# Optimization experiments

Hardware: AMD Instinct MI355X
Metric: run time of the kernel (lower is better)

## Reference

```python
import jax, jax.numpy as jnp
import numpy as np
from jax import lax

D_MODEL = 32
N_HEADS = 8
QS = 24       # query_shape
FLANGE = 8    # memory_flange


def _conv3x3(x, w, b=None):
    y = lax.conv_general_dilated(x, w, (1, 1), 'SAME',
                                 dimension_numbers=('NCHW', 'OIHW', 'NCHW'))
    if b is not None:
        y = y + b[None, :, None, None]
    return y


def _forward(x, q_w, q_b, k_w, k_b, v_w, v_b, out_w):
    B, Cin, H, W0 = x.shape
    nh, dm, qs, fl = N_HEADS, D_MODEL, QS, FLANGE
    c = dm // nh  # depth per head (=4)

    q = _conv3x3(x, q_w, q_b)
    k = _conv3x3(x, k_w, k_b)
    v = _conv3x3(x, v_w, v_b)

    pad = (-W0) % qs
    if pad:
        p = ((0, 0), (0, 0), (0, 0), (0, pad))
        q = jnp.pad(q, p); k = jnp.pad(k, p); v = jnp.pad(v, p)
    T = q.shape[-1]
    M = T // qs
    F = 2 * fl + qs  # window length (=40)

    q = q.reshape(B, nh, c, H, T) * (c ** -0.5)
    k = jnp.pad(k.reshape(B, nh, c, H, T), ((0, 0),) * 4 + ((fl, fl),))
    v = jnp.pad(v.reshape(B, nh, c, H, T), ((0, 0),) * 4 + ((fl, fl),))

    # Faithful reproduction of torch.as_strided(k, shape, unfold_q.stride()):
    # the source uses q's (contiguous, time-length T) strides on k/v whose
    # storage rows have length T+2*fl, so we gather by storage-linear index.
    s0, s1, s2, s3 = nh * c * H * T, c * H * T, H * T, T
    idx = (jnp.arange(B)[:, None, None, None, None, None] * s0
           + jnp.arange(nh)[:, None, None, None, None] * s1
           + jnp.arange(c)[:, None, None, None] * s2
           + jnp.arange(H)[:, None, None] * s3
           + jnp.arange(M)[:, None] * qs
           + jnp.arange(F))  # (B,nh,c,H,M,F)
    uk = k.reshape(-1)[idx]
    uv = v.reshape(-1)[idx]

    qq = q.reshape(B, nh, c, H, M, qs).transpose(0, 1, 4, 3, 5, 2)
    qq = qq.reshape(B * nh * M, H * qs, c)                     # (G, H*qs, c)
    k2 = uk.transpose(0, 1, 4, 2, 3, 5).reshape(B * nh * M, c, H * F)
    v2 = uv.transpose(0, 1, 4, 3, 5, 2).reshape(B * nh * M, H * F, c)

    # note: source uses -1e-09 (not -1e9); reproduced exactly
    bias = (jnp.sum(jnp.abs(k2), axis=-2, keepdims=True) == 0).astype(k2.dtype) * (-1e-09)
    weights = jax.nn.softmax(qq @ k2 + bias, axis=-1)
    o = weights @ v2                                            # (G, H*qs, c)

    o = o.reshape(B, nh, M, H, qs, c).transpose(0, 1, 5, 3, 2, 4)
    o = o.reshape(B, dm, H, M * qs)[..., :H, :W0]
    return _conv3x3(o, out_w)


def setup_inputs() -> dict:
    key = jax.random.key(0)
    ks = jax.random.split(key, 8)
    B, Cin, H, W = 2, 64, 32, 192
    s = 0.05
    return {
        'x': jax.random.normal(ks[0], (B, Cin, H, W), jnp.float32),
        'q_w': jax.random.normal(ks[1], (D_MODEL, Cin, 3, 3), jnp.float32) * s,
        'q_b': jax.random.normal(ks[2], (D_MODEL,), jnp.float32) * s,
        'k_w': jax.random.normal(ks[3], (D_MODEL, Cin, 3, 3), jnp.float32) * s,
        'k_b': jax.random.normal(ks[4], (D_MODEL,), jnp.float32) * s,
        'v_w': jax.random.normal(ks[5], (D_MODEL, Cin, 3, 3), jnp.float32) * s,
        'v_b': jax.random.normal(ks[6], (D_MODEL,), jnp.float32) * s,
        'out_w': jax.random.normal(ks[7], (64, D_MODEL, 3, 3), jnp.float32) * s,
    }


def reference(x, q_w, q_b, k_w, k_b, v_w, v_b, out_w):
    return _forward(x, q_w, q_b, k_w, k_b, v_w, v_b, out_w)
```

## Files before the change

### kernel.cpp

```cpp
#include <hip/hip_runtime.h>

namespace {
constexpr int B   = 2;
constexpr int CIN = 64;
constexpr int H   = 32;
constexpr int W   = 192;
constexpr int DM  = 32;
constexpr int NH  = 8;
constexpr int C   = 4;
constexpr int QS  = 24;
constexpr int FL  = 8;
constexpr int T   = 192;
constexpr int TP  = T + 2 * FL;
constexpr int M   = T / QS;
constexpr int F   = 2 * FL + QS;
constexpr int HF  = H * F;
constexpr int JC  = HF / 4;
constexpr int WP  = W + 2;
constexpr int HWP = H * WP;

constexpr size_t XP_OFF  = 0;
constexpr size_t KVI_OFF = 0;
constexpr size_t Q_OFF   = 1310720;
constexpr size_t K_OFF   = Q_OFF + 393216;
constexpr size_t V_OFF   = K_OFF + 425984;
constexpr size_t O_OFF   = K_OFF;
constexpr size_t ZR_OFF  = V_OFF + 425984;

constexpr int S0 = NH * C * H * T;
constexpr int S1 = C * H * T;
constexpr int S2 = H * T;
constexpr int S3 = T;
}

__global__ __launch_bounds__(256) void prep_x_k(const float* __restrict__ x,
                                                float* __restrict__ ws) {
  int row = blockIdx.x;
  int c = threadIdx.x;
  if (c >= WP) return;
  float v = (c == 0 || c == WP - 1) ? 0.f : x[(size_t)row * W + (c - 1)];
  ws[XP_OFF + (size_t)row * WP + c] = v;
}

__global__ __launch_bounds__(256) void zero_pads_k(float* __restrict__ ws) {
  int t = blockIdx.x * 256 + threadIdx.x;
  if (t < 32768) {
    int row = t >> 4;
    int p = t & 15;
    int col = (p < 8) ? p : (192 + p);
    size_t addr = (size_t)row * TP + col;
    ws[K_OFF + addr] = 0.f;
    ws[V_OFF + addr] = 0.f;
  } else if (t < 32768 + 256) {
    ws[ZR_OFF + (t - 32768)] = 0.f;
  }
}

__global__ __launch_bounds__(192) void qkv_conv_k(
    const float* __restrict__ qw, const float* __restrict__ qb,
    const float* __restrict__ kw, const float* __restrict__ kb,
    const float* __restrict__ vw, const float* __restrict__ vb,
    float* __restrict__ ws) {
  int bid = blockIdx.x;
  int y  = bid & 31;
  int co = (bid >> 5) & 31;
  int b  = bid >> 10;
  int xp = threadIdx.x;

  const float* zr  = ws + ZR_OFF;
  const float* xpb = ws + XP_OFF + (size_t)b * CIN * HWP;

  const float* p0; const float* p1; const float* p2;
  int st0, st2;
  p1 = xpb + y * WP;
  if (y > 0)     { p0 = xpb + (y - 1) * WP; st0 = HWP; } else { p0 = zr; st0 = 0; }
  if (y < H - 1) { p2 = xpb + (y + 1) * WP; st2 = HWP; } else { p2 = zr; st2 = 0; }

  const float* wq = qw + co * (CIN * 9);
  const float* wk = kw + co * (CIN * 9);
  const float* wv = vw + co * (CIN * 9);
  float aq = qb[co], ak = kb[co], av = vb[co];

#pragma unroll 2
  for (int ci = 0; ci < CIN; ++ci) {
    float a0 = p0[xp], a1 = p0[xp + 1], a2 = p0[xp + 2];
    float b0 = p1[xp], b1 = p1[xp + 1], b2 = p1[xp + 2];
    float c0 = p2[xp], c1 = p2[xp + 1], c2 = p2[xp + 2];

    aq = fmaf(a0, wq[0], aq); ak = fmaf(a0, wk[0], ak); av = fmaf(a0, wv[0], av);
    aq = fmaf(a1, wq[1], aq); ak = fmaf(a1, wk[1], ak); av = fmaf(a1, wv[1], av);
    aq = fmaf(a2, wq[2], aq); ak = fmaf(a2, wk[2], ak); av = fmaf(a2, wv[2], av);
    aq = fmaf(b0, wq[3], aq); ak = fmaf(b0, wk[3], ak); av = fmaf(b0, wv[3], av);
    aq = fmaf(b1, wq[4], aq); ak = fmaf(b1, wk[4], ak); av = fmaf(b1, wv[4], av);
    aq = fmaf(b2, wq[5], aq); ak = fmaf(b2, wk[5], ak); av = fmaf(b2, wv[5], av);
    aq = fmaf(c0, wq[6], aq); ak = fmaf(c0, wk[6], ak); av = fmaf(c0, wv[6], av);
    aq = fmaf(c1, wq[7], aq); ak = fmaf(c1, wk[7], ak); av = fmaf(c1, wv[7], av);
    aq = fmaf(c2, wq[8], aq); ak = fmaf(c2, wk[8], ak); av = fmaf(c2, wv[8], av);

    p0 += st0; p1 += HWP; p2 += st2;
    wq += 9; wk += 9; wv += 9;
  }

  ws[Q_OFF + ((size_t)(b * DM + co) * H + y) * T + xp] = aq;
  int h = co >> 2, c4 = co & 3;
  size_t pa = ((size_t)((b * NH + h) * C + c4) * H + y) * TP + FL + xp;
  ws[K_OFF + pa] = ak;
  ws[V_OFF + pa] = av;
}

__global__ __launch_bounds__(256) void build_kv_k(float* __restrict__ ws) {
  const float* kp = ws + K_OFF;
  const float* vp = ws + V_OFF;
  float* kvi = ws + KVI_OFF;
  int t = blockIdx.x * 256 + threadIdx.x;
  int c  = t & 7;
  int gj = t >> 3;
  int g  = gj / HF;
  int j  = gj - g * HF;
  int b = g >> 6, h = (g >> 3) & 7, m = g & 7;
  int hh = j / F, f = j - hh * F;
  int ci = c & 3;
  const float* src = (c < 4) ? kp : vp;
  int addr = b * S0 + h * S1 + ci * S2 + hh * S3 + m * QS + f;
  kvi[t] = src[addr];
}

__global__ __launch_bounds__(256) void attn_k(float* __restrict__ ws) {
  const float* qbuf = ws + Q_OFF;
  const float* kvi  = ws + KVI_OFF;
  float*       ob   = ws + O_OFF;

  int g  = blockIdx.x;
  int rb = blockIdx.y;
  int b = g >> 6, h = (g >> 3) & 7, m = g & 7;
  int tid = threadIdx.x;
  int row = tid & 63;
  int jc  = __builtin_amdgcn_readfirstlane(tid >> 6);

  int r  = rb * 64 + row;
  int hh = r / QS, qi = r - hh * QS;
  size_t qidx = (((size_t)(b * DM + h * C) * H + hh) * T) + m * QS + qi;
  float q0 = qbuf[qidx]             * 0.5f;
  float q1 = qbuf[qidx + H * T]     * 0.5f;
  float q2 = qbuf[qidx + 2 * H * T] * 0.5f;
  float q3 = qbuf[qidx + 3 * H * T] * 0.5f;

  const float* kvp = kvi + ((size_t)g * HF + (size_t)jc * JC) * 8;

  float s = 0.f, o0 = 0.f, o1 = 0.f, o2 = 0.f, o3 = 0.f;
#pragma unroll 4
  for (int j = 0; j < JC; ++j) {
    float4 k4 = *reinterpret_cast<const float4*>(kvp + j * 8);
    float4 v4 = *reinterpret_cast<const float4*>(kvp + j * 8 + 4);
    float l = fmaf(q0, k4.x, fmaf(q1, k4.y, fmaf(q2, k4.z, q3 * k4.w)));
    float e = __expf(l);
    s += e;
    o0 = fmaf(e, v4.x, o0);
    o1 = fmaf(e, v4.y, o1);
    o2 = fmaf(e, v4.z, o2);
    o3 = fmaf(e, v4.w, o3);
  }

  __shared__ float red[4][64][5];
  red[jc][row][0] = s;
  red[jc][row][1] = o0;
  red[jc][row][2] = o1;
  red[jc][row][3] = o2;
  red[jc][row][4] = o3;
  __syncthreads();

  if (tid < 64) {
    float S = 0.f, O0 = 0.f, O1 = 0.f, O2 = 0.f, O3 = 0.f;
#pragma unroll
    for (int cx = 0; cx < 4; ++cx) {
      S  += red[cx][tid][0];
      O0 += red[cx][tid][1];
      O1 += red[cx][tid][2];
      O2 += red[cx][tid][3];
      O3 += red[cx][tid][4];
    }
    float inv = 1.0f / S;
    size_t obase = (((size_t)(b * DM + h * C) * H + hh) * WP) + 1 + m * QS + qi;
    ob[obase]            = O0 * inv;
    ob[obase + HWP]      = O1 * inv;
    ob[obase + 2 * HWP]  = O2 * inv;
    ob[obase + 3 * HWP]  = O3 * inv;
    if (m == 0 && qi == 0) {
      ob[obase - 1] = 0.f; ob[obase - 1 + HWP] = 0.f;
      ob[obase - 1 + 2 * HWP] = 0.f; ob[obase - 1 + 3 * HWP] = 0.f;
    }
    if (m == M - 1 && qi == QS - 1) {
      ob[obase + 1] = 0.f; ob[obase + 1 + HWP] = 0.f;
      ob[obase + 1 + 2 * HWP] = 0.f; ob[obase + 1 + 3 * HWP] = 0.f;
    }
  }
}

__global__ __launch_bounds__(192) void out_conv_k(const float* __restrict__ ws,
                                                  const float* __restrict__ ow,
                                                  float* __restrict__ out) {
  int bid = blockIdx.x;
  int y  = bid & 31;
  int cq = (bid >> 5) & 15;
  int b  = bid >> 9;
  int xp = threadIdx.x;

  const float* zr  = ws + ZR_OFF;
  const float* obb = ws + O_OFF + (size_t)b * DM * HWP;

  const float* p0; const float* p1; const float* p2;
  int st0, st2;
  p1 = obb + y * WP;
  if (y > 0)     { p0 = obb + (y - 1) * WP; st0 = HWP; } else { p0 = zr; st0 = 0; }
  if (y < H - 1) { p2 = obb + (y + 1) * WP; st2 = HWP; } else { p2 = zr; st2 = 0; }

  int co0 = cq * 4;
  const float* w0 = ow + (size_t)(co0 + 0) * (DM * 9);
  const float* w1 = ow + (size_t)(co0 + 1) * (DM * 9);
  const float* w2 = ow + (size_t)(co0 + 2) * (DM * 9);
  const float* w3 = ow + (size_t)(co0 + 3) * (DM * 9);
  float A0 = 0.f, A1 = 0.f, A2 = 0.f, A3 = 0.f;

#pragma unroll 2
  for (int ci = 0; ci < DM; ++ci) {
    float a0 = p0[xp], a1 = p0[xp + 1], a2 = p0[xp + 2];
    float b0 = p1[xp], b1 = p1[xp + 1], b2 = p1[xp + 2];
    float c0 = p2[xp], c1 = p2[xp + 1], c2 = p2[xp + 2];

    A0 = fmaf(a0, w0[0], A0); A1 = fmaf(a0, w1[0], A1); A2 = fmaf(a0, w2[0], A2); A3 = fmaf(a0, w3[0], A3);
    A0 = fmaf(a1, w0[1], A0); A1 = fmaf(a1, w1[1], A1); A2 = fmaf(a1, w2[1], A2); A3 = fmaf(a1, w3[1], A3);
    A0 = fmaf(a2, w0[2], A0); A1 = fmaf(a2, w1[2], A1); A2 = fmaf(a2, w2[2], A2); A3 = fmaf(a2, w3[2], A3);
    A0 = fmaf(b0, w0[3], A0); A1 = fmaf(b0, w1[3], A1); A2 = fmaf(b0, w2[3], A2); A3 = fmaf(b0, w3[3], A3);
    A0 = fmaf(b1, w0[4], A0); A1 = fmaf(b1, w1[4], A1); A2 = fmaf(b1, w2[4], A2); A3 = fmaf(b1, w3[4], A3);
    A0 = fmaf(b2, w0[5], A0); A1 = fmaf(b2, w1[5], A1); A2 = fmaf(b2, w2[5], A2); A3 = fmaf(b2, w3[5], A3);
    A0 = fmaf(c0, w0[6], A0); A1 = fmaf(c0, w1[6], A1); A2 = fmaf(c0, w2[6], A2); A3 = fmaf(c0, w3[6], A3);
    A0 = fmaf(c1, w0[7], A0); A1 = fmaf(c1, w1[7], A1); A2 = fmaf(c1, w2[7], A2); A3 = fmaf(c1, w3[7], A3);
    A0 = fmaf(c2, w0[8], A0); A1 = fmaf(c2, w1[8], A1); A2 = fmaf(c2, w2[8], A2); A3 = fmaf(c2, w3[8], A3);

    p0 += st0; p1 += HWP; p2 += st2;
    w0 += 9; w1 += 9; w2 += 9; w3 += 9;
  }

  size_t ob0 = ((size_t)(b * 64 + co0) * H + y) * W + xp;
  out[ob0]           = A0;
  out[ob0 + H * W]   = A1;
  out[ob0 + 2*H*W]   = A2;
  out[ob0 + 3*H*W]   = A3;
}

extern "C" void kernel_launch(void* const* d_in, const int* in_sizes, int n_in,
                              void* d_out, int out_size, void* d_ws, size_t ws_size,
                              hipStream_t stream) {
  const float* x  = (const float*)d_in[0];
  const float* qw = (const float*)d_in[1];
  const float* qb = (const float*)d_in[2];
  const float* kw = (const float*)d_in[3];
  const float* kb = (const float*)d_in[4];
  const float* vw = (const float*)d_in[5];
  const float* vb = (const float*)d_in[6];
  const float* ow = (const float*)d_in[7];
  float* out = (float*)d_out;
  float* ws  = (float*)d_ws;

  hipLaunchKernelGGL(prep_x_k,   dim3(B * CIN * H), dim3(256), 0, stream, x, ws);
  hipLaunchKernelGGL(zero_pads_k, dim3(130), dim3(256), 0, stream, ws);
  hipLaunchKernelGGL(qkv_conv_k, dim3(B * 32 * 32), dim3(192), 0, stream,
                     qw, qb, kw, kb, vw, vb, ws);
  hipLaunchKernelGGL(build_kv_k, dim3(5120), dim3(256), 0, stream, ws);
  hipLaunchKernelGGL(attn_k,     dim3(128, 12), dim3(256), 0, stream, ws);
  hipLaunchKernelGGL(out_conv_k, dim3(B * 16 * 32), dim3(192), 0, stream, ws, ow, out);
}
```

Measured before the change: 117.6 us.

## Register-block conv kernels over 4 output pixels and merge prep launches

Both 3x3 conv kernels now have each thread compute four adjacent output columns. Each thread loads its input rows with float4/float2 vector reads and writes results with float4 stores. The padded row width becomes 196 so the vector loads stay aligned. The x-padding and zero-pad kernels are merged into one launch to cut launch overhead. The conv grids shrink to 512 blocks, which lowers parallelism and occupancy in exchange for reusing inputs from registers and issuing fewer memory instructions.

```diff
diff --git a/kernel.cpp b/kernel.cpp
--- a/kernel.cpp
+++ b/kernel.cpp
@@ -16,7 +16,7 @@
 constexpr int F   = 2 * FL + QS;
 constexpr int HF  = H * F;
 constexpr int JC  = HF / 4;
-constexpr int WP  = W + 2;
+constexpr int WP  = 196;
 constexpr int HWP = H * WP;
 
 constexpr size_t XP_OFF  = 0;
@@ -33,26 +33,25 @@
 constexpr int S3 = T;
 }
 
-__global__ __launch_bounds__(256) void prep_x_k(const float* __restrict__ x,
-                                                float* __restrict__ ws) {
-  int row = blockIdx.x;
-  int c = threadIdx.x;
-  if (c >= WP) return;
-  float v = (c == 0 || c == WP - 1) ? 0.f : x[(size_t)row * W + (c - 1)];
-  ws[XP_OFF + (size_t)row * WP + c] = v;
-}
-
-__global__ __launch_bounds__(256) void zero_pads_k(float* __restrict__ ws) {
-  int t = blockIdx.x * 256 + threadIdx.x;
-  if (t < 32768) {
+__global__ __launch_bounds__(256) void prep_k(const float* __restrict__ x,
+                                              float* __restrict__ ws) {
+  int bid = blockIdx.x;
+  int tid = threadIdx.x;
+  if (bid < 4096) {
+    if (tid < WP) {
+      float v = (tid >= 1 && tid <= W) ? x[(size_t)bid * W + (tid - 1)] : 0.f;
+      ws[XP_OFF + (size_t)bid * WP + tid] = v;
+    }
+  } else if (bid < 4224) {
+    int t = (bid - 4096) * 256 + tid;
     int row = t >> 4;
     int p = t & 15;
     int col = (p < 8) ? p : (192 + p);
     size_t addr = (size_t)row * TP + col;
     ws[K_OFF + addr] = 0.f;
     ws[V_OFF + addr] = 0.f;
-  } else if (t < 32768 + 256) {
-    ws[ZR_OFF + (t - 32768)] = 0.f;
+  } else {
+    ws[ZR_OFF + tid] = 0.f;
   }
 }
 
@@ -62,50 +61,67 @@
     const float* __restrict__ vw, const float* __restrict__ vb,
     float* __restrict__ ws) {
   int bid = blockIdx.x;
-  int y  = bid & 31;
-  int co = (bid >> 5) & 31;
-  int b  = bid >> 10;
-  int xp = threadIdx.x;
+  int yq = bid & 7;
+  int co = (bid >> 3) & 31;
+  int b  = bid >> 8;
+  int tid = threadIdx.x;
+  int yl = tid / 48;
+  int xq = tid - yl * 48;
+  int y  = yq * 4 + yl;
+  int xp = xq * 4;
 
   const float* zr  = ws + ZR_OFF;
   const float* xpb = ws + XP_OFF + (size_t)b * CIN * HWP;
 
-  const float* p0; const float* p1; const float* p2;
-  int st0, st2;
-  p1 = xpb + y * WP;
-  if (y > 0)     { p0 = xpb + (y - 1) * WP; st0 = HWP; } else { p0 = zr; st0 = 0; }
-  if (y < H - 1) { p2 = xpb + (y + 1) * WP; st2 = HWP; } else { p2 = zr; st2 = 0; }
+  const float* p0 = (y > 0)     ? xpb + (y - 1) * WP + xp : zr + xp;
+  const float* p1 = xpb + y * WP + xp;
+  const float* p2 = (y < H - 1) ? xpb + (y + 1) * WP + xp : zr + xp;
+  int st0 = (y > 0)     ? HWP : 0;
+  int st2 = (y < H - 1) ? HWP : 0;
 
   const float* wq = qw + co * (CIN * 9);
   const float* wk = kw + co * (CIN * 9);
   const float* wv = vw + co * (CIN * 9);
-  float aq = qb[co], ak = kb[co], av = vb[co];
+
+  float q0b = qb[co], k0b = kb[co], v0b = vb[co];
+  float Aq[4] = {q0b, q0b, q0b, q0b};
+  float Ak[4] = {k0b, k0b, k0b, k0b};
+  float Av[4] = {v0b, v0b, v0b, v0b};
 
 #pragma unroll 2
   for (int ci = 0; ci < CIN; ++ci) {
-    float a0 = p0[xp], a1 = p0[xp + 1], a2 = p0[xp + 2];
-    float b0 = p1[xp], b1 = p1[xp + 1], b2 = p1[xp + 2];
-    float c0 = p2[xp], c1 = p2[xp + 1], c2 = p2[xp + 2];
-
-    aq = fmaf(a0, wq[0], aq); ak = fmaf(a0, wk[0], ak); av = fmaf(a0, wv[0], av);
-    aq = fmaf(a1, wq[1], aq); ak = fmaf(a1, wk[1], ak); av = fmaf(a1, wv[1], av);
-    aq = fmaf(a2, wq[2], aq); ak = fmaf(a2, wk[2], ak); av = fmaf(a2, wv[2], av);
-    aq = fmaf(b0, wq[3], aq); ak = fmaf(b0, wk[3], ak); av = fmaf(b0, wv[3], av);
-    aq = fmaf(b1, wq[4], aq); ak = fmaf(b1, wk[4], ak); av = fmaf(b1, wv[4], av);
-    aq = fmaf(b2, wq[5], aq); ak = fmaf(b2, wk[5], ak); av = fmaf(b2, wv[5], av);
-    aq = fmaf(c0, wq[6], aq); ak = fmaf(c0, wk[6], ak); av = fmaf(c0, wv[6], av);
-    aq = fmaf(c1, wq[7], aq); ak = fmaf(c1, wk[7], ak); av = fmaf(c1, wv[7], av);
-    aq = fmaf(c2, wq[8], aq); ak = fmaf(c2, wk[8], ak); av = fmaf(c2, wv[8], av);
-
+    float4 a4 = *reinterpret_cast<const float4*>(p0);
+    float2 a2 = *reinterpret_cast<const float2*>(p0 + 4);
+    float4 b4 = *reinterpret_cast<const float4*>(p1);
+    float2 b2 = *reinterpret_cast<const float2*>(p1 + 4);
+    float4 c4 = *reinterpret_cast<const float4*>(p2);
+    float2 c2 = *reinterpret_cast<const float2*>(p2 + 4);
+    float av_[6] = {a4.x, a4.y, a4.z, a4.w, a2.x, a2.y};
+    float bv_[6] = {b4.x, b4.y, b4.z, b4.w, b2.x, b2.y};
+    float cv_[6] = {c4.x, c4.y, c4.z, c4.w, c2.x, c2.y};
+#pragma unroll
+    for (int dx = 0; dx < 3; ++dx) {
+      float wq0 = wq[dx], wq1 = wq[3 + dx], wq2 = wq[6 + dx];
+      float wk0 = wk[dx], wk1 = wk[3 + dx], wk2 = wk[6 + dx];
+      float wv0 = wv[dx], wv1 = wv[3 + dx], wv2 = wv[6 + dx];
+#pragma unroll
+      for (int o = 0; o < 4; ++o) {
+        float xa = av_[o + dx], xb = bv_[o + dx], xc = cv_[o + dx];
+        Aq[o] = fmaf(xa, wq0, Aq[o]); Aq[o] = fmaf(xb, wq1, Aq[o]); Aq[o] = fmaf(xc, wq2, Aq[o]);
+        Ak[o] = fmaf(xa, wk0, Ak[o]); Ak[o] = fmaf(xb, wk1, Ak[o]); Ak[o] = fmaf(xc, wk2, Ak[o]);
+        Av[o] = fmaf(xa, wv0, Av[o]); Av[o] = fmaf(xb, wv1, Av[o]); Av[o] = fmaf(xc, wv2, Av[o]);
+      }
+    }
     p0 += st0; p1 += HWP; p2 += st2;
     wq += 9; wk += 9; wv += 9;
   }
 
-  ws[Q_OFF + ((size_t)(b * DM + co) * H + y) * T + xp] = aq;
-  int h = co >> 2, c4 = co & 3;
-  size_t pa = ((size_t)((b * NH + h) * C + c4) * H + y) * TP + FL + xp;
-  ws[K_OFF + pa] = ak;
-  ws[V_OFF + pa] = av;
+  *reinterpret_cast<float4*>(ws + Q_OFF + ((size_t)(b * DM + co) * H + y) * T + xp) =
+      make_float4(Aq[0], Aq[1], Aq[2], Aq[3]);
+  int h = co >> 2, c4i = co & 3;
+  size_t pa = ((size_t)((b * NH + h) * C + c4i) * H + y) * TP + FL + xp;
+  *reinterpret_cast<float4*>(ws + K_OFF + pa) = make_float4(Ak[0], Ak[1], Ak[2], Ak[3]);
+  *reinterpret_cast<float4*>(ws + V_OFF + pa) = make_float4(Av[0], Av[1], Av[2], Av[3]);
 }
 
 __global__ __launch_bounds__(256) void build_kv_k(float* __restrict__ ws) {
@@ -200,52 +216,59 @@
                                                   const float* __restrict__ ow,
                                                   float* __restrict__ out) {
   int bid = blockIdx.x;
-  int y  = bid & 31;
-  int cq = (bid >> 5) & 15;
-  int b  = bid >> 9;
-  int xp = threadIdx.x;
+  int yq = bid & 7;
+  int cp = (bid >> 3) & 31;
+  int b  = bid >> 8;
+  int tid = threadIdx.x;
+  int yl = tid / 48;
+  int xq = tid - yl * 48;
+  int y  = yq * 4 + yl;
+  int xp = xq * 4;
 
   const float* zr  = ws + ZR_OFF;
   const float* obb = ws + O_OFF + (size_t)b * DM * HWP;
 
-  const float* p0; const float* p1; const float* p2;
-  int st0, st2;
-  p1 = obb + y * WP;
-  if (y > 0)     { p0 = obb + (y - 1) * WP; st0 = HWP; } else { p0 = zr; st0 = 0; }
-  if (y < H - 1) { p2 = obb + (y + 1) * WP; st2 = HWP; } else { p2 = zr; st2 = 0; }
-
-  int co0 = cq * 4;
-  const float* w0 = ow + (size_t)(co0 + 0) * (DM * 9);
-  const float* w1 = ow + (size_t)(co0 + 1) * (DM * 9);
-  const float* w2 = ow + (size_t)(co0 + 2) * (DM * 9);
-  const float* w3 = ow + (size_t)(co0 + 3) * (DM * 9);
-  float A0 = 0.f, A1 = 0.f, A2 = 0.f, A3 = 0.f;
+  const float* p0 = (y > 0)     ? obb + (y - 1) * WP + xp : zr + xp;
+  const float* p1 = obb + y * WP + xp;
+  const float* p2 = (y < H - 1) ? obb + (y + 1) * WP + xp : zr + xp;
+  int st0 = (y > 0)     ? HWP : 0;
+  int st2 = (y < H - 1) ? HWP : 0;
+
+  int co0 = cp * 2;
+  const float* w0 = ow + (size_t)co0 * (DM * 9);
+  const float* w1 = w0 + DM * 9;
+  float A0[4] = {0.f, 0.f, 0.f, 0.f};
+  float A1[4] = {0.f, 0.f, 0.f, 0.f};
 
 #pragma unroll 2
   for (int ci = 0; ci < DM; ++ci) {
-    float a0 = p0[xp], a1 = p0[xp + 1], a2 = p0[xp + 2];
-    float b0 = p1[xp], b1 = p1[xp + 1], b2 = p1[xp + 2];
-    float c0 = p2[xp], c1 = p2[xp + 1], c2 = p2[xp + 2];
-
-    A0 = fmaf(a0, w0[0], A0); A1 = fmaf(a0, w1[0], A1); A2 = fmaf(a0, w2[0], A2); A3 = fmaf(a0, w3[0], A3);
-    A0 = fmaf(a1, w0[1], A0); A1 = fmaf(a1, w1[1], A1); A2 = fmaf(a1, w2[1], A2); A3 = fmaf(a1, w3[1], A3);
-    A0 = fmaf(a2, w0[2], A0); A1 = fmaf(a2, w1[2], A1); A2 = fmaf(a2, w2[2], A2); A3 = fmaf(a2, w3[2], A3);
-    A0 = fmaf(b0, w0[3], A0); A1 = fmaf(b0, w1[3], A1); A2 = fmaf(b0, w2[3], A2); A3 = fmaf(b0, w3[3], A3);
-    A0 = fmaf(b1, w0[4], A0); A1 = fmaf(b1, w1[4], A1); A2 = fmaf(b1, w2[4], A2); A3 = fmaf(b1, w3[4], A3);
-    A0 = fmaf(b2, w0[5], A0); A1 = fmaf(b2, w1[5], A1); A2 = fmaf(b2, w2[5], A2); A3 = fmaf(b2, w3[5], A3);
-    A0 = fmaf(c0, w0[6], A0); A1 = fmaf(c0, w1[6], A1); A2 = fmaf(c0, w2[6], A2); A3 = fmaf(c0, w3[6], A3);
-    A0 = fmaf(c1, w0[7], A0); A1 = fmaf(c1, w1[7], A1); A2 = fmaf(c1, w2[7], A2); A3 = fmaf(c1, w3[7], A3);
-    A0 = fmaf(c2, w0[8], A0); A1 = fmaf(c2, w1[8], A1); A2 = fmaf(c2, w2[8], A2); A3 = fmaf(c2, w3[8], A3);
-
+    float4 a4 = *reinterpret_cast<const float4*>(p0);
+    float2 a2 = *reinterpret_cast<const float2*>(p0 + 4);
+    float4 b4 = *reinterpret_cast<const float4*>(p1);
+    float2 b2 = *reinterpret_cast<const float2*>(p1 + 4);
+    float4 c4 = *reinterpret_cast<const float4*>(p2);
+    float2 c2 = *reinterpret_cast<const float2*>(p2 + 4);
+    float av_[6] = {a4.x, a4.y, a4.z, a4.w, a2.x, a2.y};
+    float bv_[6] = {b4.x, b4.y, b4.z, b4.w, b2.x, b2.y};
+    float cv_[6] = {c4.x, c4.y, c4.z, c4.w, c2.x, c2.y};
+#pragma unroll
+    for (int dx = 0; dx < 3; ++dx) {
+      float u0 = w0[dx], u1 = w0[3 + dx], u2 = w0[6 + dx];
+      float t0 = w1[dx], t1 = w1[3 + dx], t2 = w1[6 + dx];
+#pragma unroll
+      for (int o = 0; o < 4; ++o) {
+        float xa = av_[o + dx], xb = bv_[o + dx], xc = cv_[o + dx];
+        A0[o] = fmaf(xa, u0, A0[o]); A0[o] = fmaf(xb, u1, A0[o]); A0[o] = fmaf(xc, u2, A0[o]);
+        A1[o] = fmaf(xa, t0, A1[o]); A1[o] = fmaf(xb, t1, A1[o]); A1[o] = fmaf(xc, t2, A1[o]);
+      }
+    }
     p0 += st0; p1 += HWP; p2 += st2;
-    w0 += 9; w1 += 9; w2 += 9; w3 += 9;
+    w0 += 9; w1 += 9;
   }
 
   size_t ob0 = ((size_t)(b * 64 + co0) * H + y) * W + xp;
-  out[ob0]           = A0;
-  out[ob0 + H * W]   = A1;
-  out[ob0 + 2*H*W]   = A2;
-  out[ob0 + 3*H*W]   = A3;
+  *reinterpret_cast<float4*>(out + ob0)         = make_float4(A0[0], A0[1], A0[2], A0[3]);
+  *reinterpret_cast<float4*>(out + ob0 + H * W) = make_float4(A1[0], A1[1], A1[2], A1[3]);
 }
 
 extern "C" void kernel_launch(void* const* d_in, const int* in_sizes, int n_in,
@@ -262,11 +285,10 @@
   float* out = (float*)d_out;
   float* ws  = (float*)d_ws;
 
-  hipLaunchKernelGGL(prep_x_k,   dim3(B * CIN * H), dim3(256), 0, stream, x, ws);
-  hipLaunchKernelGGL(zero_pads_k, dim3(130), dim3(256), 0, stream, ws);
-  hipLaunchKernelGGL(qkv_conv_k, dim3(B * 32 * 32), dim3(192), 0, stream,
+  hipLaunchKernelGGL(prep_k,     dim3(4225), dim3(256), 0, stream, x, ws);
+  hipLaunchKernelGGL(qkv_conv_k, dim3(512),  dim3(192), 0, stream,
                      qw, qb, kw, kb, vw, vb, ws);
   hipLaunchKernelGGL(build_kv_k, dim3(5120), dim3(256), 0, stream, ws);
   hipLaunchKernelGGL(attn_k,     dim3(128, 12), dim3(256), 0, stream, ws);
-  hipLaunchKernelGGL(out_conv_k, dim3(B * 16 * 32), dim3(192), 0, stream, ws, ow, out);
-}
+  hipLaunchKernelGGL(out_conv_k, dim3(512),  dim3(192), 0, stream, ws, ow, out);
+}
```

New measurement: 100.3 us. -14.7%, faster.
